# Kernel tuning notes

Measured on AMD Instinct MI355X. Metric: run time of the kernel, lower is better.

The kernel has to match this reference:

```python
import jax, jax.numpy as jnp
import numpy as np

# Dimensions: T total prefill tokens, S ragged segments (one adapter each),
# M target modules sharing this linear, r LoRA rank.
T, D_IN, D_OUT, R, M, S = 8192, 4096, 4096, 16, 2, 8


def setup_inputs() -> dict:
    key = jax.random.key(0)
    ks = jax.random.split(key, 6)
    x = jax.random.normal(ks[0], (T, D_IN), dtype=jnp.float32)
    W = jax.random.normal(ks[1], (D_OUT, D_IN), dtype=jnp.float32) * 0.02
    b = jax.random.normal(ks[2], (D_OUT,), dtype=jnp.float32) * 0.02
    # lora_A[m, s] = A.T of adapter s for target module m: [D_IN, R]
    lora_A = jax.random.normal(ks[3], (M, S, D_IN, R), dtype=jnp.float32) * 0.02
    # lora_B[m, s] = B.T: [R, D_OUT]
    lora_B = jax.random.normal(ks[4], (M, S, R, D_OUT), dtype=jnp.float32) * 0.02
    cu = jnp.sort(jax.random.randint(ks[5], (S + 1,), 0, T + 1, dtype=jnp.int32))
    cu = cu.at[0].set(0).at[-1].set(T)  # segment boundaries cover [0, T)
    return {"x": x, "W": W, "b": b, "lora_A": lora_A, "lora_B": lora_B,
            "cu_seqlen": cu}


def reference(x, W, b, lora_A, lora_B, cu_seqlen):
    # Base linear: out = x @ W.T + b
    out = x @ W.T + b
    tok = jnp.arange(x.shape[0])
    n_seg = lora_A.shape[1]
    # SGMV-style ragged LoRA: tokens in segment s use adapter s for every
    # target module m; contributions from all modules add into `out`.
    # Masking (instead of dynamic slicing) keeps shapes static / jit-friendly
    # and is exact: masked-out tokens contribute zero.
    for s in range(n_seg):
        mask = ((tok >= cu_seqlen[s]) & (tok < cu_seqlen[s + 1]))
        xm = x * mask.astype(x.dtype)[:, None]            # [T, D_IN], zero outside segment
        u = jnp.einsum('td,mdr->tmr', xm, lora_A[:, s])    # [T, M, R] low-rank down-proj
        out = out + jnp.einsum('tmr,mrD->tD', u, lora_B[:, s])  # up-proj, sum over modules
    return out
```

## Files before the change

### kernel.cpp

```cpp
#include <hip/hip_runtime.h>
#include <hip/hip_bf16.h>

#define T_TOK 8192
#define DIN   4096
#define DOUT  4096
#define RANK  16
#define NMOD  2
#define NSEG  8

typedef __attribute__((ext_vector_type(8))) short bf16x8;
typedef __attribute__((ext_vector_type(8))) unsigned short u16x8;
typedef __attribute__((ext_vector_type(4))) float f32x4;

__device__ inline unsigned short f2bf(float f) {
    union { float f; unsigned u; } v; v.f = f;
    unsigned r = v.u + 0x7FFFu + ((v.u >> 16) & 1u);
    return (unsigned short)(r >> 16);
}

__device__ inline void gload_lds16(const void* g, void* l) {
    __builtin_amdgcn_global_load_lds(
        (const __attribute__((address_space(1))) void*)g,
        (__attribute__((address_space(3))) void*)l, 16, 0, 0);
}

__global__ void cast2_bf16_kernel(const float* __restrict__ sa,
                                  unsigned short* __restrict__ da, int n8a,
                                  const float* __restrict__ sb,
                                  unsigned short* __restrict__ db, int n8b) {
    int i = blockIdx.x * blockDim.x + threadIdx.x;
    const float* s;
    unsigned short* d;
    size_t j;
    if (i < n8a) { s = sa; d = da; j = (size_t)i; }
    else if (i < n8a + n8b) { s = sb; d = db; j = (size_t)(i - n8a); }
    else return;
    const float4* s4 = (const float4*)s;
    float4 a = s4[2 * j];
    float4 b = s4[2 * j + 1];
    u16x8 o;
    o[0] = f2bf(a.x); o[1] = f2bf(a.y); o[2] = f2bf(a.z); o[3] = f2bf(a.w);
    o[4] = f2bf(b.x); o[5] = f2bf(b.y); o[6] = f2bf(b.z); o[7] = f2bf(b.w);
    *(u16x8*)(d + 8 * j) = o;
}

__global__ void prep_A_kernel(const float* __restrict__ A,
                              unsigned short* __restrict__ At) {
    int idx = blockIdx.x * 256 + threadIdx.x;
    int d   = idx & (DIN - 1);
    int smr = idx >> 12;
    int s   = smr >> 5, mr = smr & 31;
    int m   = mr >> 4,  r  = mr & 15;
    float v = A[(((size_t)(m * NSEG + s) * DIN) + d) * RANK + r];
    At[idx] = f2bf(v);
}

__global__ void prep_B_kernel(const float* __restrict__ B,
                              unsigned short* __restrict__ Bt) {
    int o  = blockIdx.x * 256 + threadIdx.x;
    int s  = o >> 12;
    int oc = o & (DOUT - 1);
    unsigned short tmp[32];
    for (int m = 0; m < NMOD; ++m)
        for (int r = 0; r < RANK; ++r)
            tmp[m * 16 + r] =
                f2bf(B[(((size_t)(m * NSEG + s) * RANK) + r) * DOUT + oc]);
    for (int k = 0; k < 4; ++k) {
        u16x8 v;
        for (int j = 0; j < 8; ++j) v[j] = tmp[k * 8 + j];
        *(u16x8*)(Bt + (size_t)o * 32 + k * 8) = v;
    }
}

__global__ __launch_bounds__(64) void u_gemm_kernel(
    const unsigned short* __restrict__ xb, const unsigned short* __restrict__ At,
    const int* __restrict__ cu, float* __restrict__ Pu) {
    int tile = blockIdx.x;
    int ky   = blockIdx.y;
    int lane = threadIdx.x;
    int l15  = lane & 15, lk = lane >> 4;
    int t0   = tile * 32;
    f32x4 acc[2][2] = {};
    bf16x8 zero = {};
    for (int s = 0; s < NSEG; ++s) {
        int lo = cu[s], hi = cu[s + 1];
        if (hi <= t0 || lo >= t0 + 32) continue;
        const unsigned short* atb = At + (size_t)(s * 32) * DIN;
        for (int kt = 0; kt < 32; ++kt) {
            int k0 = ky * 1024 + kt * 32 + lk * 8;
            bf16x8 a[2], b[2];
            for (int mi = 0; mi < 2; ++mi) {
                int row = t0 + mi * 16 + l15;
                bf16x8 av = *(const bf16x8*)(xb + (size_t)row * DIN + k0);
                a[mi] = (row >= lo && row < hi) ? av : zero;
            }
            for (int ni = 0; ni < 2; ++ni) {
                int mr = ni * 16 + l15;
                b[ni] = *(const bf16x8*)(atb + (size_t)mr * DIN + k0);
            }
            for (int mi = 0; mi < 2; ++mi)
                for (int ni = 0; ni < 2; ++ni)
                    acc[mi][ni] = __builtin_amdgcn_mfma_f32_16x16x32_bf16(
                        a[mi], b[ni], acc[mi][ni], 0, 0, 0);
        }
    }
    for (int mi = 0; mi < 2; ++mi)
        for (int ni = 0; ni < 2; ++ni)
            for (int j = 0; j < 4; ++j) {
                int t  = t0 + mi * 16 + lk * 4 + j;
                int mr = ni * 16 + l15;
                Pu[((size_t)ky * T_TOK + t) * 32 + mr] = acc[mi][ni][j];
            }
}

__global__ void reduce_u_kernel(const float* __restrict__ Pu,
                                unsigned short* __restrict__ ub) {
    int idx = blockIdx.x * 256 + threadIdx.x;
    const size_t STRIDE = (size_t)T_TOK * 32;
    float s = Pu[idx] + Pu[idx + STRIDE] + Pu[idx + 2 * STRIDE] + Pu[idx + 3 * STRIDE];
    ub[idx] = f2bf(s);
}


__device__ __forceinline__ bf16x8 lds_frag(const char* tile, int row, int lk) {
    int rb = (row << 6) + (lk << 4);
    rb ^= ((rb >> 7) & 7) << 4;
    return *(const bf16x8*)(tile + rb);
}

__device__ __forceinline__ void stage_chunk(const unsigned short* gbase,
                                            char* lds_tile, int chunkbase, int tid) {
    int tb = chunkbase + tid * 16;
    int gb = tb ^ (((tb >> 7) & 7) << 4);
    int row = gb >> 6;
    int col = (gb & 63) >> 1;
    gload_lds16(gbase + (size_t)row * DIN + col, lds_tile + tb);
}

#define STAGE(T_)                                                              \
  {                                                                            \
    int k0s_ = (T_) * 32;                                                      \
    char* dst_ = lds + ((T_) & 3) * 32768;                                     \
    stage_chunk(xrow + k0s_, dst_, 0, tid);                                    \
    stage_chunk(xrow + k0s_, dst_, 8192, tid);                                 \
    stage_chunk(wrow_g + k0s_, dst_ + 16384, 0, tid);                          \
    stage_chunk(wrow_g + k0s_, dst_ + 16384, 8192, tid);                       \
  }

#define READ_AF2(T_)                                                           \
  {                                                                            \
    const char* Asl_ = lds + ((T_) & 3) * 32768;                               \
    for (int m = 0; m < 4; ++m)                                                \
        af2[m] = lds_frag(Asl_, wrow + (4 + m) * 16 + l15, lk);                \
  }

#define READ_MAIN(BFR_, AF_, T_)                                               \
  {                                                                            \
    const char* Asl_ = lds + ((T_) & 3) * 32768;                               \
    const char* Bsl_ = Asl_ + 16384;                                           \
    for (int n = 0; n < 4; ++n)                                                \
        BFR_[n] = lds_frag(Bsl_, wcol + n * 16 + l15, lk);                     \
    for (int m = 0; m < 4; ++m)                                                \
        AF_[m] = lds_frag(Asl_, wrow + m * 16 + l15, lk);                      \
  }

#define CLUSTER(BFR_, AF_)                                                     \
  {                                                                            \
    __builtin_amdgcn_s_setprio(1);                                             \
    for (int m = 0; m < 4; ++m)                                                \
        for (int n = 0; n < 4; ++n)                                            \
            acc[m][n] = __builtin_amdgcn_mfma_f32_16x16x32_bf16(               \
                AF_[m], BFR_[n], acc[m][n], 0, 0, 0);                          \
    for (int m = 0; m < 4; ++m)                                                \
        for (int n = 0; n < 4; ++n)                                            \
            acc[4 + m][n] = __builtin_amdgcn_mfma_f32_16x16x32_bf16(           \
                af2[m], BFR_[n], acc[4 + m][n], 0, 0, 0);                      \
    __builtin_amdgcn_s_setprio(0);                                             \
  }

#define ITER(UB_, UA_, RB_, RA_, T_, STG_, VM_)                                \
  {                                                                            \
    READ_AF2(T_);                                                              \
    READ_MAIN(RB_, RA_, (T_) + 1);                                             \
    if (STG_) STAGE((T_) + 3);                                                 \
    __builtin_amdgcn_sched_barrier(0);                                         \
    CLUSTER(UB_, UA_);                                                         \
    if ((VM_) == 4)      asm volatile("s_waitcnt vmcnt(4)" ::: "memory");      \
    else if ((VM_) == 0) asm volatile("s_waitcnt vmcnt(0)" ::: "memory");      \
    if ((VM_) >= 0) __builtin_amdgcn_s_barrier();                              \
  }

__global__ __launch_bounds__(512, 2) void main_gemm_kernel(
    const unsigned short* __restrict__ xb, const unsigned short* __restrict__ wb,
    const unsigned short* __restrict__ ub, const unsigned short* __restrict__ bt,
    const float* __restrict__ bias, const int* __restrict__ cu,
    float* __restrict__ out) {
    __shared__ __attribute__((aligned(1024))) char lds[131072];
    int tid  = threadIdx.x;
    int w    = tid >> 6, lane = tid & 63;
    int l15  = lane & 15, lk = lane >> 4;
    int wrow = (w >> 2) * 128;
    int wcol = (w & 3) * 64;
    int swz  = (blockIdx.x & 7) * 64 + (blockIdx.x >> 3);
    int row0 = (swz >> 4) * 256;
    int col0 = (swz & 15) * 256;

    const unsigned short* xrow   = xb + (size_t)row0 * DIN;
    const unsigned short* wrow_g = wb + (size_t)col0 * DIN;

    f32x4 acc[8][4] = {};
    bf16x8 bfrA[4], afA[4], bfrB[4], afB[4], af2[4];

    STAGE(0); STAGE(1); STAGE(2);
    asm volatile("s_waitcnt vmcnt(4)" ::: "memory");
    __builtin_amdgcn_s_barrier();
    READ_MAIN(bfrA, afA, 0);

    #pragma unroll 1
    for (int t = 0; t < 124; t += 2) {
        ITER(bfrA, afA, bfrB, afB, t,     1, 4);
        ITER(bfrB, afB, bfrA, afA, t + 1, 1, 4);
    }
    ITER(bfrA, afA, bfrB, afB, 124, 1, 4);
    ITER(bfrB, afB, bfrA, afA, 125, 0, 0);
    ITER(bfrA, afA, bfrB, afB, 126, 0, -1);
    { READ_AF2(127); __builtin_amdgcn_sched_barrier(0); CLUSTER(bfrB, afB); }

    bf16x8 zero = {};
    for (int s = 0; s < NSEG; ++s) {
        int lo = cu[s], hi = cu[s + 1];
        if (hi <= row0 || lo >= row0 + 256) continue;
        bf16x8 au[8], bu[4];
        for (int m = 0; m < 8; ++m) {
            int row = row0 + wrow + m * 16 + l15;
            bf16x8 v = *(const bf16x8*)(ub + (size_t)row * 32 + lk * 8);
            au[m] = (row >= lo && row < hi) ? v : zero;
        }
        for (int n = 0; n < 4; ++n) {
            int col = col0 + wcol + n * 16 + l15;
            bu[n] = *(const bf16x8*)(bt + ((size_t)s * DOUT + col) * 32 + lk * 8);
        }
        for (int m = 0; m < 8; ++m)
            for (int n = 0; n < 4; ++n)
                acc[m][n] = __builtin_amdgcn_mfma_f32_16x16x32_bf16(
                    au[m], bu[n], acc[m][n], 0, 0, 0);
    }

    float bv[4];
    for (int n = 0; n < 4; ++n) bv[n] = bias[col0 + wcol + n * 16 + l15];
    for (int m = 0; m < 8; ++m) {
        int rbase = row0 + wrow + m * 16 + lk * 4;
        for (int n = 0; n < 4; ++n) {
            int col = col0 + wcol + n * 16 + l15;
            for (int jj = 0; jj < 4; ++jj)
                out[(size_t)(rbase + jj) * DOUT + col] = acc[m][n][jj] + bv[n];
        }
    }
}

extern "C" void kernel_launch(void* const* d_in, const int* in_sizes, int n_in,
                              void* d_out, int out_size, void* d_ws, size_t ws_size,
                              hipStream_t stream) {
    const float* x  = (const float*)d_in[0];
    const float* W  = (const float*)d_in[1];
    const float* b  = (const float*)d_in[2];
    const float* lA = (const float*)d_in[3];
    const float* lB = (const float*)d_in[4];
    const int*   cu = (const int*)d_in[5];
    float* out = (float*)d_out;

    char* ws = (char*)d_ws;
    unsigned short* xb = (unsigned short*)(ws);
    unsigned short* wb = (unsigned short*)(ws + 67108864);
    unsigned short* At = (unsigned short*)(ws + 100663296);
    unsigned short* Bt = (unsigned short*)(ws + 102760448);
    float*          Pu = (float*)(ws + 104857600);
    unsigned short* ub = (unsigned short*)(ws + 109051904);

    const int n8x = T_TOK * DIN / 8, n8w = DOUT * DIN / 8;
    cast2_bf16_kernel<<<(n8x + n8w) / 256, 256, 0, stream>>>(x, xb, n8x, W, wb, n8w);
    prep_A_kernel<<<(NSEG * 32 * DIN) / 256, 256, 0, stream>>>(lA, At);
    prep_B_kernel<<<(NSEG * DOUT) / 256, 256, 0, stream>>>(lB, Bt);
    dim3 ug(T_TOK / 32, 4);
    u_gemm_kernel<<<ug, 64, 0, stream>>>(xb, At, cu, Pu);
    reduce_u_kernel<<<(T_TOK * 32) / 256, 256, 0, stream>>>(Pu, ub);
    dim3 mg(32 * 16);
    main_gemm_kernel<<<mg, 512, 0, stream>>>(xb, wb, ub, Bt, b, cu, out);
}
```

Before: 326.6 us.

## Restructure main GEMM to 128x256 tiles with 256 threads and 3-stage LDS ring

Replaces the 256x256 tile / 512-thread main GEMM with a 128x256 tile / 256-thread block, where each wave covers all 128 rows and 64 columns. It uses a triple-buffered LDS ring of 24KB per stage instead of four 32KB stages, a new XOR swizzle, and splits each k-step into two MFMA halves with the global-to-LDS staging interleaved between them. The grid doubles to 1024 blocks with a new block-order swizzle. The goal is better latency hiding and more blocks in flight per CU. The cost is more barriers per k-step, lower reuse of W per block, and more total global traffic for W.

```diff
diff --git a/kernel.cpp b/kernel.cpp
--- a/kernel.cpp
+++ b/kernel.cpp
@@ -122,117 +122,108 @@
 }
 
 
-__device__ __forceinline__ bf16x8 lds_frag(const char* tile, int row, int lk) {
-    int rb = (row << 6) + (lk << 4);
-    rb ^= ((rb >> 7) & 7) << 4;
-    return *(const bf16x8*)(tile + rb);
-}
-
-__device__ __forceinline__ void stage_chunk(const unsigned short* gbase,
-                                            char* lds_tile, int chunkbase, int tid) {
-    int tb = chunkbase + tid * 16;
-    int gb = tb ^ (((tb >> 7) & 7) << 4);
-    int row = gb >> 6;
-    int col = (gb & 63) >> 1;
-    gload_lds16(gbase + (size_t)row * DIN + col, lds_tile + tb);
-}
-
-#define STAGE(T_)                                                              \
-  {                                                                            \
-    int k0s_ = (T_) * 32;                                                      \
-    char* dst_ = lds + ((T_) & 3) * 32768;                                     \
-    stage_chunk(xrow + k0s_, dst_, 0, tid);                                    \
-    stage_chunk(xrow + k0s_, dst_, 8192, tid);                                 \
-    stage_chunk(wrow_g + k0s_, dst_ + 16384, 0, tid);                          \
-    stage_chunk(wrow_g + k0s_, dst_ + 16384, 8192, tid);                       \
-  }
-
-#define READ_AF2(T_)                                                           \
-  {                                                                            \
-    const char* Asl_ = lds + ((T_) & 3) * 32768;                               \
-    for (int m = 0; m < 4; ++m)                                                \
-        af2[m] = lds_frag(Asl_, wrow + (4 + m) * 16 + l15, lk);                \
-  }
-
-#define READ_MAIN(BFR_, AF_, T_)                                               \
-  {                                                                            \
-    const char* Asl_ = lds + ((T_) & 3) * 32768;                               \
-    const char* Bsl_ = Asl_ + 16384;                                           \
-    for (int n = 0; n < 4; ++n)                                                \
-        BFR_[n] = lds_frag(Bsl_, wcol + n * 16 + l15, lk);                     \
-    for (int m = 0; m < 4; ++m)                                                \
-        AF_[m] = lds_frag(Asl_, wrow + m * 16 + l15, lk);                      \
-  }
-
-#define CLUSTER(BFR_, AF_)                                                     \
-  {                                                                            \
+__device__ __forceinline__ bf16x8 fragA(const char* mat, int row, int lk) {
+    int rb = (row << 6) + ((lk ^ ((row >> 1) & 3)) << 4);
+    return *(const bf16x8*)(mat + rb);
+}
+
+#define STAGE_R(GB_, LD_, TB_, K0_)                                           \
+  { int tb = (TB_);                                                            \
+    int lrow = tb >> 6;                                                        \
+    int cb = (tb & 63) ^ (((lrow >> 1) & 3) << 4);                             \
+    gload_lds16((GB_) + (size_t)lrow * DIN + (K0_) + (cb >> 1), (LD_) + tb); }
+
+#define MFMA16(B0_, AF_)                                                       \
     __builtin_amdgcn_s_setprio(1);                                             \
     for (int m = 0; m < 4; ++m)                                                \
         for (int n = 0; n < 4; ++n)                                            \
-            acc[m][n] = __builtin_amdgcn_mfma_f32_16x16x32_bf16(               \
-                AF_[m], BFR_[n], acc[m][n], 0, 0, 0);                          \
-    for (int m = 0; m < 4; ++m)                                                \
-        for (int n = 0; n < 4; ++n)                                            \
-            acc[4 + m][n] = __builtin_amdgcn_mfma_f32_16x16x32_bf16(           \
-                af2[m], BFR_[n], acc[4 + m][n], 0, 0, 0);                      \
-    __builtin_amdgcn_s_setprio(0);                                             \
+            acc[(B0_) + m][n] = __builtin_amdgcn_mfma_f32_16x16x32_bf16(       \
+                AF_[m], bf[n], acc[(B0_) + m][n], 0, 0, 0);                    \
+    __builtin_amdgcn_s_setprio(0);
+
+#define PH_MID()                                                               \
+    __builtin_amdgcn_s_barrier();                                              \
+    asm volatile("s_waitcnt lgkmcnt(0)" ::: "memory");                         \
+    __builtin_amdgcn_sched_barrier(0);
+
+#define BODY(T_, SR_, SS_, STG_, VM_)                                          \
+  {                                                                            \
+    const char* cA = lds + (SR_) * 24576;                                      \
+    const char* cB = cA + 8192;                                                \
+    char* sA = lds + (SS_) * 24576;                                            \
+    char* sB = sA + 8192;                                                      \
+    const int k0n = ((T_) + 2) * 32;                                           \
+    bf16x8 bf[4], af[4];                                                       \
+                                             \
+    for (int n = 0; n < 4; ++n) bf[n] = fragA(cB, wcol + n*16 + l15, lk);      \
+    for (int m = 0; m < 4; ++m) af[m] = fragA(cA, m*16 + l15, lk);             \
+    if (STG_) { STAGE_R(xrow, sA, tid*16, k0n);                                \
+                STAGE_R(xrow, sA, 4096 + tid*16, k0n);                         \
+                STAGE_R(wrow_g, sB, tid*16, k0n); }                            \
+    PH_MID();                                                                  \
+    MFMA16(0, af);                                                             \
+    __builtin_amdgcn_s_barrier();                                              \
+                                             \
+    for (int m = 0; m < 4; ++m) af[m] = fragA(cA, 64 + m*16 + l15, lk);        \
+    if (STG_) { STAGE_R(wrow_g, sB, 4096 + tid*16, k0n);                       \
+                STAGE_R(wrow_g, sB, 8192 + tid*16, k0n);                       \
+                STAGE_R(wrow_g, sB, 12288 + tid*16, k0n); }                    \
+    if ((VM_) == 6)      asm volatile("s_waitcnt vmcnt(6)" ::: "memory");      \
+    else if ((VM_) == 0) asm volatile("s_waitcnt vmcnt(0)" ::: "memory");      \
+    PH_MID();                                                                  \
+    MFMA16(4, af);                                                             \
+    __builtin_amdgcn_s_barrier();                                              \
   }
 
-#define ITER(UB_, UA_, RB_, RA_, T_, STG_, VM_)                                \
-  {                                                                            \
-    READ_AF2(T_);                                                              \
-    READ_MAIN(RB_, RA_, (T_) + 1);                                             \
-    if (STG_) STAGE((T_) + 3);                                                 \
-    __builtin_amdgcn_sched_barrier(0);                                         \
-    CLUSTER(UB_, UA_);                                                         \
-    if ((VM_) == 4)      asm volatile("s_waitcnt vmcnt(4)" ::: "memory");      \
-    else if ((VM_) == 0) asm volatile("s_waitcnt vmcnt(0)" ::: "memory");      \
-    if ((VM_) >= 0) __builtin_amdgcn_s_barrier();                              \
-  }
-
-__global__ __launch_bounds__(512, 2) void main_gemm_kernel(
+__global__ __launch_bounds__(256, 2) void main_gemm_kernel(
     const unsigned short* __restrict__ xb, const unsigned short* __restrict__ wb,
     const unsigned short* __restrict__ ub, const unsigned short* __restrict__ bt,
     const float* __restrict__ bias, const int* __restrict__ cu,
     float* __restrict__ out) {
-    __shared__ __attribute__((aligned(1024))) char lds[131072];
+    __shared__ __attribute__((aligned(1024))) char lds[73728];
     int tid  = threadIdx.x;
     int w    = tid >> 6, lane = tid & 63;
     int l15  = lane & 15, lk = lane >> 4;
-    int wrow = (w >> 2) * 128;
-    int wcol = (w & 3) * 64;
-    int swz  = (blockIdx.x & 7) * 64 + (blockIdx.x >> 3);
-    int row0 = (swz >> 4) * 256;
-    int col0 = (swz & 15) * 256;
+    int wcol = w * 64;
+    int swz  = (blockIdx.x & 7) * 128 + (blockIdx.x >> 3);
+    int colp = swz >> 6;
+    int rowp = swz & 63;
+    int row0 = rowp * 128, col0 = colp * 256;
 
     const unsigned short* xrow   = xb + (size_t)row0 * DIN;
     const unsigned short* wrow_g = wb + (size_t)col0 * DIN;
 
     f32x4 acc[8][4] = {};
-    bf16x8 bfrA[4], afA[4], bfrB[4], afB[4], af2[4];
-
-    STAGE(0); STAGE(1); STAGE(2);
-    asm volatile("s_waitcnt vmcnt(4)" ::: "memory");
+
+    {
+        char* sA = lds;          char* sB = lds + 8192;
+        STAGE_R(xrow, sA, tid*16, 0);  STAGE_R(xrow, sA, 4096 + tid*16, 0);
+        STAGE_R(wrow_g, sB, tid*16, 0); STAGE_R(wrow_g, sB, 4096 + tid*16, 0);
+        STAGE_R(wrow_g, sB, 8192 + tid*16, 0); STAGE_R(wrow_g, sB, 12288 + tid*16, 0);
+        sA = lds + 24576;        sB = sA + 8192;
+        STAGE_R(xrow, sA, tid*16, 32); STAGE_R(xrow, sA, 4096 + tid*16, 32);
+        STAGE_R(wrow_g, sB, tid*16, 32); STAGE_R(wrow_g, sB, 4096 + tid*16, 32);
+        STAGE_R(wrow_g, sB, 8192 + tid*16, 32); STAGE_R(wrow_g, sB, 12288 + tid*16, 32);
+    }
+    asm volatile("s_waitcnt vmcnt(6)" ::: "memory");
     __builtin_amdgcn_s_barrier();
-    READ_MAIN(bfrA, afA, 0);
 
     #pragma unroll 1
-    for (int t = 0; t < 124; t += 2) {
-        ITER(bfrA, afA, bfrB, afB, t,     1, 4);
-        ITER(bfrB, afB, bfrA, afA, t + 1, 1, 4);
-    }
-    ITER(bfrA, afA, bfrB, afB, 124, 1, 4);
-    ITER(bfrB, afB, bfrA, afA, 125, 0, 0);
-    ITER(bfrA, afA, bfrB, afB, 126, 0, -1);
-    { READ_AF2(127); __builtin_amdgcn_sched_barrier(0); CLUSTER(bfrB, afB); }
+    for (int t = 0; t < 126; t += 3) {
+        BODY(t,     0, 2, 1, 6);
+        BODY(t + 1, 1, 0, 1, 6);
+        BODY(t + 2, 2, 1, 1, 6);
+    }
+    BODY(126, 0, 2, 0, 0);
+    BODY(127, 1, 2, 0, -1);
 
     bf16x8 zero = {};
     for (int s = 0; s < NSEG; ++s) {
         int lo = cu[s], hi = cu[s + 1];
-        if (hi <= row0 || lo >= row0 + 256) continue;
+        if (hi <= row0 || lo >= row0 + 128) continue;
         bf16x8 au[8], bu[4];
         for (int m = 0; m < 8; ++m) {
-            int row = row0 + wrow + m * 16 + l15;
+            int row = row0 + m * 16 + l15;
             bf16x8 v = *(const bf16x8*)(ub + (size_t)row * 32 + lk * 8);
             au[m] = (row >= lo && row < hi) ? v : zero;
         }
@@ -249,7 +240,7 @@
     float bv[4];
     for (int n = 0; n < 4; ++n) bv[n] = bias[col0 + wcol + n * 16 + l15];
     for (int m = 0; m < 8; ++m) {
-        int rbase = row0 + wrow + m * 16 + lk * 4;
+        int rbase = row0 + m * 16 + lk * 4;
         for (int n = 0; n < 4; ++n) {
             int col = col0 + wcol + n * 16 + l15;
             for (int jj = 0; jj < 4; ++jj)
@@ -284,6 +275,6 @@
     dim3 ug(T_TOK / 32, 4);
     u_gemm_kernel<<<ug, 64, 0, stream>>>(xb, At, cu, Pu);
     reduce_u_kernel<<<(T_TOK * 32) / 256, 256, 0, stream>>>(Pu, ub);
-    dim3 mg(32 * 16);
-    main_gemm_kernel<<<mg, 512, 0, stream>>>(xb, wb, ub, Bt, b, cu, out);
-}
+    dim3 mg(64 * 16);
+    main_gemm_kernel<<<mg, 256, 0, stream>>>(xb, wb, ub, Bt, b, cu, out);
+}
```

After: 351.8 us. +7.7%, slower.
